# Optimization experiments

Measured on AMD Instinct MI355X. Metric: run time of the kernel, lower is better.

## Reference

```python
import jax, jax.numpy as jnp
import numpy as np

B, S, H, D, P = 16, 512, 12, 768, 256
TOP_RATE = 0.1
K = int(round(TOP_RATE * S))  # 51, matches round(self.top_rate * hidden_state.size(1))
LN_EPS = 1e-5


def setup_inputs() -> dict:
    key = jax.random.key(0)
    ks = jax.random.split(key, 6)
    return {
        "hidden_state": jax.random.normal(ks[0], (B, S, D), dtype=jnp.float32),
        "attention": jax.random.normal(ks[1], (B, H, S, S), dtype=jnp.float32),
        "length": S,  # uniform valid length (scalar int)
        # node_trans: Linear(D, P)
        "W_node": jax.random.normal(ks[2], (D, P), dtype=jnp.float32) * 0.02,
        "b_node": jnp.zeros((P,), dtype=jnp.float32),
        # node_eta parameter, initialized to 0 (self.node_eta.data.fill_(0))
        "node_eta": jnp.zeros((1,), dtype=jnp.float32),
        # fc: Linear(P, P)
        "W_fc": jax.random.normal(ks[3], (P, P), dtype=jnp.float32) * 0.02,
        "b_fc": jnp.zeros((P,), dtype=jnp.float32),
        # LayerNorm(P)
        "ln_gamma": jnp.ones((P,), dtype=jnp.float32),
        "ln_beta": jnp.zeros((P,), dtype=jnp.float32),
    }


def reference(hidden_state, attention, W_node, b_node, node_eta, W_fc, b_fc,
              ln_gamma, ln_beta, length):
    # average attention over heads: [B, S, S]
    avg_atten = attention.mean(axis=1)
    # per-target-node top-k neighbors
    vals, idx = jax.lax.top_k(avg_atten, K)  # [B, S, K]
    # edge mask replicating softmax(where(v>0, v, -1e9)) followed by nonzero():
    # entries at -1e9 underflow to exactly 0 in fp32 softmax iff the row has a
    # positive value; otherwise the softmax is uniform and all edges survive.
    keep = vals > 0.0
    row_has_pos = keep.any(axis=-1, keepdims=True)
    keep = jnp.where(row_has_pos, keep, True)            # [B, S, K] (>=1 True per row)
    keepf = keep.astype(hidden_state.dtype)[..., None]   # [B, S, K, 1]

    # node_trans on all nodes: [B, S, P]
    h = hidden_state @ W_node + b_node

    # gather source-node features h[b, idx[b, t, j], :] -> [B, S, K, P]
    gathered = jax.vmap(lambda hb, ib: hb[ib])(h, idx)

    # reduce='mean': edge weight w=1, mailbox mean over kept incoming edges
    h_agg = (gathered * keepf).sum(axis=2) / keepf.sum(axis=2)

    eta = node_eta[0]
    new_h = eta * h + (1.0 - eta) * h_agg                # [B, S, P]

    # dgl.mean_nodes: mean over the `length` nodes of each sub-graph (=S here)
    out = new_h.mean(axis=1)                             # [B, P]

    # fc(dropout(tanh(out))) with dropout in eval mode (identity)
    out = jnp.tanh(out) @ W_fc + b_fc

    # LayerNorm
    mu = out.mean(axis=-1, keepdims=True)
    var = ((out - mu) ** 2).mean(axis=-1, keepdims=True)
    out = (out - mu) / jnp.sqrt(var + LN_EPS) * ln_gamma + ln_beta
    return out
```

## Files before the change

kernel.cpp:

```cpp
#include <hip/hip_runtime.h>
#include <math.h>

#define B_ 16
#define S_ 512
#define H_ 12
#define D_ 768
#define P_ 256
#define K_ 51
#define CH_ 16
#define NCHUNK_ (S_/CH_)

__device__ __forceinline__ unsigned okey(float f) {
  unsigned u = __float_as_uint(f);
  return (u & 0x80000000u) ? ~u : (u | 0x80000000u);
}

__global__ __launch_bounds__(256) void k1_topk_mask(
    const float* __restrict__ attn, unsigned long long* __restrict__ maskbuf,
    float* __restrict__ invbuf) {
  const int tid = threadIdx.x;
  const int wv = tid >> 6;
  const int lane = tid & 63;
  const int bt = blockIdx.x * 4 + wv;
  const int b = bt >> 9;
  const int t = bt & (S_ - 1);

  const float* base = attn + (((size_t)b * H_) * S_ + t) * S_;
  float a[8] = {0.f, 0.f, 0.f, 0.f, 0.f, 0.f, 0.f, 0.f};
  #pragma unroll
  for (int h = 0; h < H_; ++h) {
    const float* r = base + (size_t)h * (S_ * S_);
    const float4 u = *(const float4*)(r + 4 * lane);
    const float4 v = *(const float4*)(r + 256 + 4 * lane);
    a[0] += u.x; a[1] += u.y; a[2] += u.z; a[3] += u.w;
    a[4] += v.x; a[5] += v.y; a[6] += v.z; a[7] += v.w;
  }
  unsigned k[8];
  #pragma unroll
  for (int i = 0; i < 8; ++i) {
    a[i] *= (1.0f / (float)H_);
    k[i] = okey(a[i]);
  }

  int p = 0;
  #pragma unroll
  for (int i = 0; i < 8; ++i) p += __popcll(__ballot(a[i] > 0.f));

  bool sel[8];
  float invcnt;
  if (p >= 1 && p < K_) {
    #pragma unroll
    for (int i = 0; i < 8; ++i) sel[i] = (a[i] > 0.f);
    invcnt = 1.0f / (float)p;
  } else {
    unsigned prefix = 0;
    int rem = K_;
    bool done = false;
    unsigned dmask = 0, thr = 0;
    for (int bpos = 31; bpos >= 0; --bpos) {
      const unsigned bit = 1u << bpos;
      const unsigned mb = ~(bit - 1u);
      const unsigned cand = prefix | bit;
      int cnt = 0;
      #pragma unroll
      for (int i = 0; i < 8; ++i)
        cnt += __popcll(__ballot((k[i] & mb) == cand));
      if (cnt == rem) { done = true; dmask = mb; thr = cand; break; }
      if (cnt > rem) prefix = cand;
      else rem -= cnt;
    }
    if (done) {
      #pragma unroll
      for (int i = 0; i < 8; ++i) sel[i] = (k[i] & dmask) >= thr;
    } else {
      const unsigned T = prefix;
      unsigned long long mm[8];
      #pragma unroll
      for (int i = 0; i < 8; ++i) mm[i] = __ballot(k[i] == T);
      const unsigned long long lt = ((unsigned long long)1 << lane) - 1ull;
      int fh = 0;
      #pragma unroll
      for (int i = 0; i < 4; ++i) fh += __popcll(mm[i]);
      #pragma unroll
      for (int i = 0; i < 8; ++i) {
        sel[i] = (k[i] > T);
        if (k[i] == T) {
          int r = 0;
          if (i < 4) {
            #pragma unroll
            for (int i2 = 0; i2 < 4; ++i2) r += __popcll(mm[i2] & lt);
            for (int i2 = 0; i2 < i; ++i2) r += (int)((mm[i2] >> lane) & 1ull);
          } else {
            r = fh;
            #pragma unroll
            for (int i2 = 4; i2 < 8; ++i2) r += __popcll(mm[i2] & lt);
            for (int i2 = 4; i2 < i; ++i2) r += (int)((mm[i2] >> lane) & 1ull);
          }
          if (r < rem) sel[i] = true;
        }
      }
    }
    invcnt = 1.0f / (float)K_;
  }

  unsigned long long m[8];
  #pragma unroll
  for (int i = 0; i < 8; ++i) m[i] = __ballot(sel[i]);
  if (lane == 0) {
    ulonglong2* mp = (ulonglong2*)(maskbuf + (size_t)bt * 8);
    mp[0] = ulonglong2{m[0], m[1]};
    mp[1] = ulonglong2{m[2], m[3]};
    mp[2] = ulonglong2{m[4], m[5]};
    mp[3] = ulonglong2{m[6], m[7]};
    invbuf[bt] = invcnt;
  }
}

__global__ __launch_bounds__(256) void k1b_colsum(
    const unsigned long long* __restrict__ maskbuf,
    const float* __restrict__ invbuf, const float* __restrict__ node_eta,
    float* __restrict__ coef) {
  const int half = blockIdx.x;
  const int b = blockIdx.y;
  const int tid = threadIdx.x;
  __shared__ unsigned long long ms[S_][8];
  __shared__ float inv[S_];

  const ulonglong2* mrow2 = (const ulonglong2*)(maskbuf + (size_t)b * S_ * 8);
  ulonglong2* lds2 = (ulonglong2*)&ms[0][0];
  #pragma unroll
  for (int j = 0; j < 8; ++j) lds2[tid + 256 * j] = mrow2[tid + 256 * j];
  inv[tid] = invbuf[b * S_ + tid];
  inv[tid + 256] = invbuf[b * S_ + tid + 256];
  __syncthreads();

  const int s = half * 256 + tid;
  const int wi = (s < 256) ? (s & 3) : 4 + (s & 3);
  const unsigned long long bitm = 1ull << ((s & 255) >> 2);
  float w = 0.f;
  #pragma unroll 8
  for (int tt = 0; tt < S_; ++tt)
    if (ms[tt][wi] & bitm) w += inv[tt];

  const float eta = node_eta[0];
  coef[b * S_ + s] = (eta + (1.0f - eta) * w) * (1.0f / (float)S_);
}

__global__ __launch_bounds__(192) void k2_weighted_sum(
    const float* __restrict__ hidden, const float* __restrict__ coef,
    float* __restrict__ x) {
  const int chunk = blockIdx.x;
  const int b = blockIdx.y;
  const int tid = threadIdx.x;
  __shared__ float cs[CH_];
  if (tid < CH_) cs[tid] = coef[b * S_ + chunk * CH_ + tid];
  __syncthreads();
  const float* hb = hidden + ((size_t)b * S_ + (size_t)chunk * CH_) * D_ + 4 * tid;
  float4 acc = make_float4(0.f, 0.f, 0.f, 0.f);
  #pragma unroll
  for (int s = 0; s < CH_; ++s) {
    const float4 v = *(const float4*)(hb + (size_t)s * D_);
    const float c = cs[s];
    acc.x += c * v.x; acc.y += c * v.y; acc.z += c * v.z; acc.w += c * v.w;
  }
  float* xp = x + b * D_ + 4 * tid;
  atomicAdd(xp + 0, acc.x);
  atomicAdd(xp + 1, acc.y);
  atomicAdd(xp + 2, acc.z);
  atomicAdd(xp + 3, acc.w);
}

__global__ __launch_bounds__(256) void k3a_tanh_matvec(
    const float* __restrict__ x, const float* __restrict__ W_node,
    const float* __restrict__ b_node, float* __restrict__ tbuf) {
  const int j = blockIdx.x;
  const int b = blockIdx.y;
  const int tid = threadIdx.x;
  const int pp = tid & 15;
  const int g = tid >> 4;
  __shared__ float xs[D_];
  __shared__ float part[16][32];
  for (int d = tid; d < D_; d += 256) xs[d] = x[b * D_ + d];
  __syncthreads();
  const float* Wp = W_node + 32 * j + 2 * pp;
  float2 acc = make_float2(0.f, 0.f);
  const int d0 = 48 * g;
  #pragma unroll 8
  for (int dd = 0; dd < 48; ++dd) {
    const int d = d0 + dd;
    const float2 wv = *(const float2*)(Wp + (size_t)d * P_);
    const float xv = xs[d];
    acc.x += xv * wv.x; acc.y += xv * wv.y;
  }
  *(float2*)&part[g][2 * pp] = acc;
  __syncthreads();
  if (tid < 32) {
    float s = 0.f;
    #pragma unroll
    for (int gg = 0; gg < 16; ++gg) s += part[gg][tid];
    const int pcol = 32 * j + tid;
    tbuf[b * P_ + pcol] = tanhf(s + b_node[pcol]);
  }
}

__global__ __launch_bounds__(256) void k3bc_fc_ln(
    const float* __restrict__ tbuf, const float* __restrict__ W_fc,
    const float* __restrict__ b_fc, const float* __restrict__ gamma,
    const float* __restrict__ beta, float* __restrict__ out) {
  const int b = blockIdx.x;
  const int tid = threadIdx.x;
  __shared__ float ts[P_];
  __shared__ float red[4];
  ts[tid] = tbuf[b * P_ + tid];
  __syncthreads();
  float acc = 0.f;
  #pragma unroll 8
  for (int q = 0; q < P_; ++q) acc += ts[q] * W_fc[(size_t)q * P_ + tid];
  const float o = acc + b_fc[tid];

  float s = o;
  #pragma unroll
  for (int off = 32; off > 0; off >>= 1) s += __shfl_down(s, off, 64);
  const int wave = tid >> 6, lane = tid & 63;
  if (lane == 0) red[wave] = s;
  __syncthreads();
  const float mu = (red[0] + red[1] + red[2] + red[3]) * (1.0f / (float)P_);
  __syncthreads();
  const float dv = o - mu;
  float s2 = dv * dv;
  #pragma unroll
  for (int off = 32; off > 0; off >>= 1) s2 += __shfl_down(s2, off, 64);
  if (lane == 0) red[wave] = s2;
  __syncthreads();
  const float var = (red[0] + red[1] + red[2] + red[3]) * (1.0f / (float)P_);
  const float inv = 1.0f / sqrtf(var + 1e-5f);
  out[b * P_ + tid] = dv * inv * gamma[tid] + beta[tid];
}

extern "C" void kernel_launch(void* const* d_in, const int* in_sizes, int n_in,
                              void* d_out, int out_size, void* d_ws, size_t ws_size,
                              hipStream_t stream) {
  (void)in_sizes; (void)n_in; (void)out_size; (void)ws_size;
  const float* hidden   = (const float*)d_in[0];
  const float* attn     = (const float*)d_in[1];
  const float* W_node   = (const float*)d_in[3];
  const float* b_node   = (const float*)d_in[4];
  const float* node_eta = (const float*)d_in[5];
  const float* W_fc     = (const float*)d_in[6];
  const float* b_fc     = (const float*)d_in[7];
  const float* gamma    = (const float*)d_in[8];
  const float* beta     = (const float*)d_in[9];
  float* out = (float*)d_out;

  unsigned long long* maskbuf = (unsigned long long*)d_ws;
  float* invbuf = (float*)(maskbuf + (size_t)B_ * S_ * 8);
  float* coef   = invbuf + B_ * S_;
  float* x      = coef + B_ * S_;
  float* tbuf   = x + B_ * D_;

  hipMemsetAsync(x, 0, (size_t)(B_ * D_) * sizeof(float), stream);

  k1_topk_mask<<<(B_ * S_) / 4, 256, 0, stream>>>(attn, maskbuf, invbuf);
  k1b_colsum<<<dim3(2, B_), 256, 0, stream>>>(maskbuf, invbuf, node_eta, coef);
  k2_weighted_sum<<<dim3(NCHUNK_, B_), 192, 0, stream>>>(hidden, coef, x);
  k3a_tanh_matvec<<<dim3(8, B_), 256, 0, stream>>>(x, W_node, b_node, tbuf);
  k3bc_fc_ln<<<B_, 256, 0, stream>>>(tbuf, W_fc, b_fc, gamma, beta, out);
}
```

Before: 378.1 us.

## Fuse colsum into weighted sum and merge tail kernels, drop atomics

Result: no change. 382.9 us (+1.3%).

```diff
diff --git a/kernel.cpp b/kernel.cpp
--- a/kernel.cpp
+++ b/kernel.cpp
@@ -116,45 +116,49 @@
   }
 }
 
-__global__ __launch_bounds__(256) void k1b_colsum(
+__global__ __launch_bounds__(192) void k2_colsum_wsum(
     const unsigned long long* __restrict__ maskbuf,
     const float* __restrict__ invbuf, const float* __restrict__ node_eta,
-    float* __restrict__ coef) {
-  const int half = blockIdx.x;
-  const int b = blockIdx.y;
-  const int tid = threadIdx.x;
-  __shared__ unsigned long long ms[S_][8];
-  __shared__ float inv[S_];
-
-  const ulonglong2* mrow2 = (const ulonglong2*)(maskbuf + (size_t)b * S_ * 8);
-  ulonglong2* lds2 = (ulonglong2*)&ms[0][0];
-  #pragma unroll
-  for (int j = 0; j < 8; ++j) lds2[tid + 256 * j] = mrow2[tid + 256 * j];
-  inv[tid] = invbuf[b * S_ + tid];
-  inv[tid + 256] = invbuf[b * S_ + tid + 256];
-  __syncthreads();
-
-  const int s = half * 256 + tid;
-  const int wi = (s < 256) ? (s & 3) : 4 + (s & 3);
-  const unsigned long long bitm = 1ull << ((s & 255) >> 2);
-  float w = 0.f;
-  #pragma unroll 8
-  for (int tt = 0; tt < S_; ++tt)
-    if (ms[tt][wi] & bitm) w += inv[tt];
-
-  const float eta = node_eta[0];
-  coef[b * S_ + s] = (eta + (1.0f - eta) * w) * (1.0f / (float)S_);
-}
-
-__global__ __launch_bounds__(192) void k2_weighted_sum(
-    const float* __restrict__ hidden, const float* __restrict__ coef,
-    float* __restrict__ x) {
+    const float* __restrict__ hidden, float* __restrict__ x_part) {
   const int chunk = blockIdx.x;
   const int b = blockIdx.y;
   const int tid = threadIdx.x;
+  __shared__ unsigned long long ld[S_ * 4];
+  __shared__ float inv[S_];
+  __shared__ float part[16][8];
   __shared__ float cs[CH_];
-  if (tid < CH_) cs[tid] = coef[b * S_ + chunk * CH_ + tid];
-  __syncthreads();
+
+  const int wi0 = (chunk < 16) ? 0 : 4;
+  for (int i = tid; i < S_ * 4; i += 192) {
+    const int t = i >> 2, j = i & 3;
+    ld[i] = maskbuf[(((size_t)b << 9) + t) * 8 + wi0 + j];
+  }
+  for (int i = tid; i < S_; i += 192) inv[i] = invbuf[(b << 9) + i];
+  __syncthreads();
+
+  if (tid < 128) {
+    const int c = tid >> 3, g = tid & 7;
+    const int s = chunk * CH_ + c;
+    const int j = s & 3;
+    const unsigned long long bm = 1ull << ((s & 255) >> 2);
+    float w = 0.f;
+    #pragma unroll 8
+    for (int i = 0; i < 64; ++i) {
+      const int t = i * 8 + g;
+      if (ld[t * 4 + j] & bm) w += inv[t];
+    }
+    part[c][g] = w;
+  }
+  __syncthreads();
+  if (tid < CH_) {
+    float w = 0.f;
+    #pragma unroll
+    for (int g = 0; g < 8; ++g) w += part[tid][g];
+    const float eta = node_eta[0];
+    cs[tid] = (eta + (1.0f - eta) * w) * (1.0f / (float)S_);
+  }
+  __syncthreads();
+
   const float* hb = hidden + ((size_t)b * S_ + (size_t)chunk * CH_) * D_ + 4 * tid;
   float4 acc = make_float4(0.f, 0.f, 0.f, 0.f);
   #pragma unroll
@@ -163,60 +167,40 @@
     const float c = cs[s];
     acc.x += c * v.x; acc.y += c * v.y; acc.z += c * v.z; acc.w += c * v.w;
   }
-  float* xp = x + b * D_ + 4 * tid;
-  atomicAdd(xp + 0, acc.x);
-  atomicAdd(xp + 1, acc.y);
-  atomicAdd(xp + 2, acc.z);
-  atomicAdd(xp + 3, acc.w);
-}
-
-__global__ __launch_bounds__(256) void k3a_tanh_matvec(
-    const float* __restrict__ x, const float* __restrict__ W_node,
-    const float* __restrict__ b_node, float* __restrict__ tbuf) {
-  const int j = blockIdx.x;
-  const int b = blockIdx.y;
-  const int tid = threadIdx.x;
-  const int pp = tid & 15;
-  const int g = tid >> 4;
-  __shared__ float xs[D_];
-  __shared__ float part[16][32];
-  for (int d = tid; d < D_; d += 256) xs[d] = x[b * D_ + d];
-  __syncthreads();
-  const float* Wp = W_node + 32 * j + 2 * pp;
-  float2 acc = make_float2(0.f, 0.f);
-  const int d0 = 48 * g;
-  #pragma unroll 8
-  for (int dd = 0; dd < 48; ++dd) {
-    const int d = d0 + dd;
-    const float2 wv = *(const float2*)(Wp + (size_t)d * P_);
-    const float xv = xs[d];
-    acc.x += xv * wv.x; acc.y += xv * wv.y;
-  }
-  *(float2*)&part[g][2 * pp] = acc;
-  __syncthreads();
-  if (tid < 32) {
-    float s = 0.f;
-    #pragma unroll
-    for (int gg = 0; gg < 16; ++gg) s += part[gg][tid];
-    const int pcol = 32 * j + tid;
-    tbuf[b * P_ + pcol] = tanhf(s + b_node[pcol]);
-  }
-}
-
-__global__ __launch_bounds__(256) void k3bc_fc_ln(
-    const float* __restrict__ tbuf, const float* __restrict__ W_fc,
+  *(float4*)(x_part + ((size_t)chunk * B_ + b) * D_ + 4 * tid) = acc;
+}
+
+__global__ __launch_bounds__(256) void k3_tail(
+    const float* __restrict__ x_part, const float* __restrict__ W_node,
+    const float* __restrict__ b_node, const float* __restrict__ W_fc,
     const float* __restrict__ b_fc, const float* __restrict__ gamma,
     const float* __restrict__ beta, float* __restrict__ out) {
   const int b = blockIdx.x;
   const int tid = threadIdx.x;
+  __shared__ float xs[D_];
   __shared__ float ts[P_];
   __shared__ float red[4];
-  ts[tid] = tbuf[b * P_ + tid];
-  __syncthreads();
+
+  #pragma unroll
+  for (int d = tid; d < D_; d += 256) {
+    float s = 0.f;
+    #pragma unroll 8
+    for (int c = 0; c < NCHUNK_; ++c)
+      s += x_part[((size_t)c * B_ + b) * D_ + d];
+    xs[d] = s;
+  }
+  __syncthreads();
+
   float acc = 0.f;
   #pragma unroll 8
-  for (int q = 0; q < P_; ++q) acc += ts[q] * W_fc[(size_t)q * P_ + tid];
-  const float o = acc + b_fc[tid];
+  for (int d = 0; d < D_; ++d) acc += xs[d] * W_node[(size_t)d * P_ + tid];
+  ts[tid] = tanhf(acc + b_node[tid]);
+  __syncthreads();
+
+  float o = 0.f;
+  #pragma unroll 8
+  for (int q = 0; q < P_; ++q) o += ts[q] * W_fc[(size_t)q * P_ + tid];
+  o += b_fc[tid];
 
   float s = o;
   #pragma unroll
@@ -254,15 +238,11 @@
 
   unsigned long long* maskbuf = (unsigned long long*)d_ws;
   float* invbuf = (float*)(maskbuf + (size_t)B_ * S_ * 8);
-  float* coef   = invbuf + B_ * S_;
-  float* x      = coef + B_ * S_;
-  float* tbuf   = x + B_ * D_;
-
-  hipMemsetAsync(x, 0, (size_t)(B_ * D_) * sizeof(float), stream);
+  float* x_part = invbuf + B_ * S_;
 
   k1_topk_mask<<<(B_ * S_) / 4, 256, 0, stream>>>(attn, maskbuf, invbuf);
-  k1b_colsum<<<dim3(2, B_), 256, 0, stream>>>(maskbuf, invbuf, node_eta, coef);
-  k2_weighted_sum<<<dim3(NCHUNK_, B_), 192, 0, stream>>>(hidden, coef, x);
-  k3a_tanh_matvec<<<dim3(8, B_), 256, 0, stream>>>(x, W_node, b_node, tbuf);
-  k3bc_fc_ln<<<B_, 256, 0, stream>>>(tbuf, W_fc, b_fc, gamma, beta, out);
-}
+  k2_colsum_wsum<<<dim3(NCHUNK_, B_), 192, 0, stream>>>(maskbuf, invbuf,
+                                                        node_eta, hidden, x_part);
+  k3_tail<<<B_, 256, 0, stream>>>(x_part, W_node, b_node, W_fc, b_fc,
+                                  gamma, beta, out);
+}
```
